# Kernel tuning notes

Measured on AMD Instinct MI355X. Metric: run time of the kernel, lower is better.

## Reference

```python
import jax, jax.numpy as jnp
import numpy as np

IN_F, HID, OUT_F = 227, 1024, 227
BATCH, SEQ_LEN = 256, 100
COND_NUM, GT_NUM = 5, 5


def _condition_lst(seq_len, condition_num=COND_NUM, groundtruth_num=GT_NUM):
    gt = np.ones((100, groundtruth_num))
    con = np.zeros((100, condition_num))
    lst = np.concatenate((gt, con), 1).reshape(-1)
    return lst[:seq_len].astype(bool)


def _lstm_cell(x, h, c, Wih, Whh, bih, bhh):
    gates = x @ Wih.T + bih + h @ Whh.T + bhh  # [B, 4H]
    i, f, g, o = jnp.split(gates, 4, axis=-1)
    c_new = jax.nn.sigmoid(f) * c + jax.nn.sigmoid(i) * jnp.tanh(g)
    h_new = jax.nn.sigmoid(o) * jnp.tanh(c_new)
    return h_new, c_new


def setup_inputs() -> dict:
    key = jax.random.key(0)
    ks = jax.random.split(key, 16)
    s = 0.03
    inp = {"real_seq": jax.random.normal(ks[0], (BATCH, SEQ_LEN, IN_F), jnp.float32)}
    shapes = {
        "Wih1": (4 * HID, IN_F), "Whh1": (4 * HID, HID), "bih1": (4 * HID,), "bhh1": (4 * HID,),
        "Wih2": (4 * HID, HID), "Whh2": (4 * HID, HID), "bih2": (4 * HID,), "bhh2": (4 * HID,),
        "Wih3": (4 * HID, HID), "Whh3": (4 * HID, HID), "bih3": (4 * HID,), "bhh3": (4 * HID,),
        "Wd": (OUT_F, HID), "bd": (OUT_F,),
    }
    for i, (name, shp) in enumerate(shapes.items()):
        inp[name] = jax.random.normal(ks[i + 1], shp, jnp.float32) * s
    return inp


def reference(real_seq, Wih1, Whh1, bih1, bhh1, Wih2, Whh2, bih2, bhh2,
              Wih3, Whh3, bih3, bhh3, Wd, bd):
    batch, seq_len, _ = real_seq.shape
    cond = jnp.asarray(_condition_lst(seq_len))  # [T] bool, True -> teacher forcing
    zeros_h = jnp.zeros((batch, HID), real_seq.dtype)
    out0 = jnp.zeros((batch, OUT_F), real_seq.dtype)
    carry0 = (zeros_h, zeros_h, zeros_h, zeros_h, zeros_h, zeros_h, out0)

    def step(carry, xs):
        h0, h1, h2, c0, c1, c2, prev_out = carry
        gt_frame, use_gt = xs
        in_frame = jnp.where(use_gt, gt_frame, prev_out)
        # NOTE: faithful to the original quirk — lstm2/lstm3 consume the OLD
        # h0 / h1 (pre-update), not the freshly computed ones.
        h0n, c0n = _lstm_cell(in_frame, h0, c0, Wih1, Whh1, bih1, bhh1)
        h1n, c1n = _lstm_cell(h0, h1, c1, Wih2, Whh2, bih2, bhh2)
        h2n, c2n = _lstm_cell(h1, h2, c2, Wih3, Whh3, bih3, bhh3)
        out_frame = h2n @ Wd.T + bd
        return (h0n, h1n, h2n, c0n, c1n, c2n, out_frame), out_frame

    xs = (jnp.transpose(real_seq, (1, 0, 2)), cond)  # [T,B,F], [T]
    _, out_frames = jax.lax.scan(step, carry0, xs)   # [T,B,OUT_F]
    out_seq = jnp.transpose(out_frames, (1, 0, 2)).reshape(batch, seq_len * OUT_F)
    return out_seq
```

## Files before the change

### kernel.cpp

```cpp
#include <hip/hip_runtime.h>
#include <cstdint>

typedef _Float16 f16;
typedef _Float16 f16x8 __attribute__((ext_vector_type(8)));
typedef float    f32x4 __attribute__((ext_vector_type(4)));

#define DINL __device__ __forceinline__

static constexpr int HID = 1024;
static constexpr int NG  = 4096;
static constexpr int BB  = 256;
static constexpr int TT  = 100;
static constexpr int KX  = 256;
static constexpr size_t MSZ = (size_t)NG * HID;

static constexpr size_t OFF_PACKW5 = 0;
static constexpr size_t OFF_W1D    = OFF_PACKW5 + 5*MSZ*2;
static constexpr size_t OFF_WIH1   = OFF_W1D   + MSZ*2;
static constexpr size_t OFF_WD     = OFF_WIH1  + (size_t)NG*KX*2;
static constexpr size_t OFF_XPAD   = OFF_WD    + (size_t)256*HID*2;
static constexpr size_t OFF_BIAS   = OFF_XPAD  + (size_t)TT*BB*KX*2;
static constexpr size_t OFF_C      = OFF_BIAS  + (size_t)4*NG*4;
static constexpr size_t OFF_HBUF   = OFF_C     + (size_t)3*BB*HID*4;
static constexpr size_t OFF_H2Z    = OFF_HBUF  + (size_t)4*BB*HID*2;
static constexpr size_t OFF_H2ALL  = OFF_H2Z   + (size_t)BB*HID*2;

DINL void async16(void* lds, const void* g){
  auto lp = reinterpret_cast<__attribute__((address_space(3))) unsigned int*>(
      reinterpret_cast<uintptr_t>(lds));
  auto gp = reinterpret_cast<const __attribute__((address_space(1))) unsigned int*>(
      reinterpret_cast<uintptr_t>(g));
  __builtin_amdgcn_global_load_lds(gp, lp, 16, 0, 0);
}

DINL f16x8 ldsr128(unsigned a){
  f16x8 r;
  asm volatile("ds_read_b128 %0, %1" : "=v"(r) : "v"(a));
  return r;
}

DINL float sigf(float x){
  x = fminf(fmaxf(x, -30.f), 30.f);
  return __fdividef(1.f, 1.f + __expf(-x));
}
DINL float tanh_fast(float x){
  x = fminf(fmaxf(x, -15.f), 15.f);
  float t = __expf(2.f*x);
  return __fdividef(t - 1.f, t + 1.f);
}

DINL void gemm_tile(f32x4 acc[4][4],
                    const f16* __restrict__ A, int m0, int sA,
                    const f16* __restrict__ Bp, int n0, int K,
                    char* ldsA, char* ldsB, int w, int lane)
{
  const int m_w = (w>>1)*64, n_w = (w&1)*64, c15 = lane&15;
  for (int k0 = 0; k0 < K; k0 += 64){
    __syncthreads();
    #pragma unroll
    for (int q = 0; q < 4; q++){
      int r0  = w*32 + q*8;
      int row = r0 + (lane>>3);
      int kg  = (lane&7) ^ (row&7);
      async16(ldsA + r0*128, A  + (size_t)(m0+row)*sA + k0 + kg*8);
      async16(ldsB + r0*128, Bp + (size_t)(n0+row)*K  + k0 + kg*8);
    }
    __syncthreads();
    #pragma unroll
    for (int kw = 0; kw < 2; kw++){
      f16x8 af[4], bf[4];
      #pragma unroll
      for (int ti = 0; ti < 4; ti++){
        int row  = m_w + ti*16 + c15;
        int phys = (kw*4 + (lane>>4)) ^ (row&7);
        af[ti] = *(const f16x8*)(ldsA + row*128 + phys*16);
      }
      #pragma unroll
      for (int tj = 0; tj < 4; tj++){
        int row  = n_w + tj*16 + c15;
        int phys = (kw*4 + (lane>>4)) ^ (row&7);
        bf[tj] = *(const f16x8*)(ldsB + row*128 + phys*16);
      }
      #pragma unroll
      for (int ti = 0; ti < 4; ti++)
        #pragma unroll
        for (int tj = 0; tj < 4; tj++)
          acc[ti][tj] = __builtin_amdgcn_mfma_f32_16x16x32_f16(af[ti], bf[tj], acc[ti][tj], 0, 0, 0);
    }
  }
}


__global__ void k_pack5(const float* W0, const float* W1, const float* W2,
                        const float* W3, const float* W4, char* ws)
{
  f16* dst = (f16*)(ws + OFF_PACKW5);
  const int mat = blockIdx.y;
  const float* src = mat==0?W0 : mat==1?W1 : mat==2?W2 : mat==3?W3 : W4;
  int tid = blockIdx.x*256 + threadIdx.x;
  int n = tid >> 7, kc = tid & 127;
  int r = ((n&3) << 10) + (n >> 2);
  const float* s = src + (size_t)r*HID + kc*8;
  f16x8 o;
  #pragma unroll
  for (int i = 0; i < 8; i++) o[i] = (f16)s[i];
  *(f16x8*)(dst + (size_t)mat*MSZ + (size_t)n*HID + kc*8) = o;
}

__global__ void k_packwih1(const float* __restrict__ Wih1, char* ws){
  f16* dst = (f16*)(ws + OFF_WIH1);
  int n = blockIdx.x, k = threadIdx.x;
  int r = ((n&3) << 10) + (n >> 2);
  dst[(size_t)n*KX + k] = (k < 227) ? (f16)Wih1[(size_t)r*227 + k] : (f16)0.f;
}

__global__ void k_packwd(const float* __restrict__ Wd, char* ws){
  f16* dst = (f16*)(ws + OFF_WD);
  int o = blockIdx.x;
  #pragma unroll
  for (int j = 0; j < 4; j++){
    int k = threadIdx.x + j*256;
    dst[(size_t)o*HID + k] = (o < 227) ? (f16)Wd[(size_t)o*HID + k] : (f16)0.f;
  }
}

__global__ void k_packwdt(const float* __restrict__ Wd, char* ws){
  f16* dst = (f16*)(ws + OFF_H2ALL);
  int h = blockIdx.x, o = threadIdx.x;
  dst[(size_t)h*KX + o] = (o < 227) ? (f16)Wd[(size_t)o*HID + h] : (f16)0.f;
}

__global__ void k_xpad(const float* __restrict__ seq, char* ws){
  f16* dst = (f16*)(ws + OFF_XPAD);
  int idx = blockIdx.x*256 + threadIdx.x;
  int t = idx >> 16, rem = idx & 65535, b = rem >> 8, k = rem & 255;
  dst[idx] = (k < 227) ? (f16)seq[(size_t)b*22700 + (size_t)t*227 + k] : (f16)0.f;
}

__global__ void k_bias(const float* bih1, const float* bhh1, const float* bih2, const float* bhh2,
                       const float* bih3, const float* bhh3, const float* Wih1, const float* bd,
                       char* ws)
{
  int n = blockIdx.x*256 + threadIdx.x;
  if (n >= NG) return;
  int r = ((n&3) << 10) + (n >> 2);
  float* b = (float*)(ws + OFF_BIAS);
  float bf = bih1[r] + bhh1[r];
  float s = 0.f;
  for (int o = 0; o < 227; o++) s += Wih1[(size_t)r*227 + o] * bd[o];
  b[n]        = bf;
  b[NG + n]   = bf + s;
  b[2*NG + n] = bih2[r] + bhh2[r];
  b[3*NG + n] = bih3[r] + bhh3[r];
}

__global__ __launch_bounds__(256, 2) void k_w1d(char* ws)
{
  __shared__ __align__(16) char ldsA[16384];
  __shared__ __align__(16) char ldsB[16384];
  const int w = threadIdx.x >> 6, lane = threadIdx.x & 63;
  const int n0 = blockIdx.x*128, m0 = blockIdx.y*128;
  const f16* A  = (const f16*)(ws + OFF_WIH1);
  const f16* Bp = (const f16*)(ws + OFF_H2ALL);
  f16* W1D = (f16*)(ws + OFF_W1D);

  f32x4 acc[4][4];
  f32x4 zero = {0.f, 0.f, 0.f, 0.f};
  #pragma unroll
  for (int i = 0; i < 4; i++)
    #pragma unroll
    for (int j = 0; j < 4; j++) acc[i][j] = zero;

  gemm_tile(acc, A, m0, KX, Bp, n0, KX, ldsA, ldsB, w, lane);

  const int m_w = (w>>1)*64, n_w = (w&1)*64, quad = lane>>4, c15 = lane&15;
  #pragma unroll
  for (int tj = 0; tj < 4; tj++){
    int col = n0 + n_w + tj*16 + c15;
    #pragma unroll
    for (int ti = 0; ti < 4; ti++){
      f32x4 v = acc[ti][tj];
      #pragma unroll
      for (int r = 0; r < 4; r++){
        int m = m0 + m_w + ti*16 + quad*4 + r;
        W1D[(size_t)m*HID + col] = (f16)v[r];
      }
    }
  }
}

__global__ __launch_bounds__(512, 2) void k_step(char* __restrict__ ws, int t, int use_gt)
{
  __shared__ __align__(16) char lds[163840];
  const int w = threadIdx.x >> 6, lane = threadIdx.x & 63;
  const int col0 = blockIdx.x*64, layer = blockIdx.y;

  const f16* packW = (const f16*)(ws + OFF_PACKW5);
  const f16* W1D   = (const f16*)(ws + OFF_W1D);
  const f16* WIH1  = (const f16*)(ws + OFF_WIH1);
  const f16* XP    = (const f16*)(ws + OFF_XPAD) + (size_t)t*BB*KX;
  const float* biasb = (const float*)(ws + OFF_BIAS);
  float* Cst = (float*)(ws + OFF_C);
  f16* HB  = (f16*)(ws + OFF_HBUF);
  f16* H2Z = (f16*)(ws + OFF_H2Z);
  f16* H2A = (f16*)(ws + OFF_H2ALL);

  const int pr = t & 1, pw = pr ^ 1;
  const f16* h0p = HB + (size_t)(pr*2 + 0)*BB*HID;
  const f16* h1p = HB + (size_t)(pr*2 + 1)*BB*HID;
  const f16* h2p = (t == 0) ? H2Z : (H2A + (size_t)(t-1)*BB*HID);

  const f16 *A0, *A1, *B0, *B1; int K1, sA1;
  const float* biasp; f16* hout; float* cptr;
  if (layer == 0){
    A0 = h0p; B0 = packW;
    if (use_gt){ A1 = XP;  B1 = WIH1; K1 = KX;  sA1 = KX;  biasp = biasb; }
    else       { A1 = h2p; B1 = W1D;  K1 = HID; sA1 = HID; biasp = biasb + NG; }
    hout = HB + (size_t)(pw*2 + 0)*BB*HID; cptr = Cst;
  } else if (layer == 1){
    A0 = h0p; B0 = packW + MSZ;  A1 = h1p; B1 = packW + 2*MSZ; K1 = HID; sA1 = HID;
    biasp = biasb + 2*NG; hout = HB + (size_t)(pw*2 + 1)*BB*HID; cptr = Cst + (size_t)BB*HID;
  } else {
    A0 = h1p; B0 = packW + 3*MSZ; A1 = h2p; B1 = packW + 4*MSZ; K1 = HID; sA1 = HID;
    biasp = biasb + 3*NG; hout = H2A + (size_t)t*BB*HID; cptr = Cst + (size_t)2*BB*HID;
  }
  const int ncmax = 16 + (K1 >> 6);

  const int rsub = lane >> 3;
  const int kxe  = ((lane & 7) ^ rsub) * 8;

  auto issueA = [&](int cc, int buf){
    const f16* src; int strd;
    if (cc < 16){ src = A0 + (size_t)cc*64;      strd = HID; }
    else        { src = A1 + (size_t)(cc-16)*64; strd = sA1; }
    char* dst = lds + 65536 + w*12288 + buf*4096;
    #pragma unroll
    for (int q = 0; q < 4; q++)
      async16(dst + q*1024, src + (size_t)(w*32 + q*8 + rsub)*strd + kxe);
  };
  auto issueB = [&](int chunk, int j){
    const f16* src; int strd;
    if (chunk < 16){ src = B0 + (size_t)chunk*64;      strd = HID; }
    else           { src = B1 + (size_t)(chunk-16)*64; strd = K1;  }
    async16(lds + (chunk & 7)*8192 + j*1024,
            src + (size_t)(col0 + j*8 + rsub)*strd + kxe);
  };

  f32x4 acc[2][4];
  f32x4 zero = {0.f, 0.f, 0.f, 0.f};
  #pragma unroll
  for (int i = 0; i < 2; i++)
    #pragma unroll
    for (int j = 0; j < 4; j++) acc[i][j] = zero;

  const int m_w = w*32, c15 = lane&15, quad = lane>>4;

  const unsigned ldsBase = (unsigned)(uintptr_t)lds;
  const unsigned p0 = (unsigned)(( quad      ^ (c15&7)) * 16);
  const unsigned p1 = (unsigned)(((4 + quad) ^ (c15&7)) * 16);
  unsigned rA[2], rB[4];
  #pragma unroll
  for (int ti = 0; ti < 2; ti++) rA[ti] = (unsigned)((ti*16 + c15) * 128);
  #pragma unroll
  for (int tj = 0; tj < 4; tj++) rB[tj] = (unsigned)((tj*16 + c15) * 128);

  {
    const int cb = w >> 1, jb = (w & 1) * 4;
    #pragma unroll
    for (int k = 0; k < 4; k++) issueB(cb, jb + k);
  }
  issueA(0, 0); issueA(1, 1);

  int bR = 0, bW = 2;
  for (int c = 0; c < ncmax; c++){
    if (c == ncmax-1)                    asm volatile("s_waitcnt vmcnt(0)" ::: "memory");
    else if ((c&3)==0 || c >= ncmax-4)   asm volatile("s_waitcnt vmcnt(4)" ::: "memory");
    else                                 asm volatile("s_waitcnt vmcnt(5)" ::: "memory");
    if ((c & 3) == 0) __builtin_amdgcn_s_barrier();
    if (c <= ncmax-5) issueB(4*((c>>2)+1) + (w>>1), (w&1)*4 + (c&3));
    if (c <= ncmax-3) issueA(c+2, bW);

    const unsigned ab = ldsBase + 65536u + (unsigned)(w*12288) + (unsigned)(bR*4096);
    const unsigned bb = ldsBase + (unsigned)((c & 7) * 8192);

    f16x8 a0[2], b0[4], a1[2], b1[4];
    #pragma unroll
    for (int ti = 0; ti < 2; ti++) a0[ti] = ldsr128(ab + rA[ti] + p0);
    #pragma unroll
    for (int tj = 0; tj < 4; tj++) b0[tj] = ldsr128(bb + rB[tj] + p0);
    #pragma unroll
    for (int ti = 0; ti < 2; ti++) a1[ti] = ldsr128(ab + rA[ti] + p1);
    #pragma unroll
    for (int tj = 0; tj < 4; tj++) b1[tj] = ldsr128(bb + rB[tj] + p1);

    asm volatile("s_waitcnt lgkmcnt(6)"
      : "+v"(a0[0]), "+v"(a0[1]),
        "+v"(b0[0]), "+v"(b0[1]), "+v"(b0[2]), "+v"(b0[3]));
    #pragma unroll
    for (int ti = 0; ti < 2; ti++)
      #pragma unroll
      for (int tj = 0; tj < 4; tj++)
        acc[ti][tj] = __builtin_amdgcn_mfma_f32_16x16x32_f16(a0[ti], b0[tj], acc[ti][tj], 0, 0, 0);

    asm volatile("s_waitcnt lgkmcnt(0)"
      : "+v"(a1[0]), "+v"(a1[1]),
        "+v"(b1[0]), "+v"(b1[1]), "+v"(b1[2]), "+v"(b1[3]));
    #pragma unroll
    for (int ti = 0; ti < 2; ti++)
      #pragma unroll
      for (int tj = 0; tj < 4; tj++)
        acc[ti][tj] = __builtin_amdgcn_mfma_f32_16x16x32_f16(a1[ti], b1[tj], acc[ti][tj], 0, 0, 0);

    bR = (bR == 2) ? 0 : bR + 1;
    bW = (bW == 2) ? 0 : bW + 1;
  }

  const int gl = lane&3, sbase = lane&60;
  #pragma unroll
  for (int tj = 0; tj < 4; tj++){
    const int ncol = col0 + tj*16 + c15;
    const int unit = ncol >> 2;
    const float bn = biasp[ncol];
    float cp[8];
    #pragma unroll
    for (int ti = 0; ti < 2; ti++)
      #pragma unroll
      for (int r = 0; r < 4; r++)
        cp[ti*4 + r] = cptr[(size_t)(m_w + ti*16 + quad*4 + r)*HID + unit];
    #pragma unroll
    for (int ti = 0; ti < 2; ti++){
      f32x4 v = acc[ti][tj];
      #pragma unroll
      for (int r = 0; r < 4; r++){
        float x   = v[r] + bn;
        float act = (gl == 2) ? tanh_fast(x) : sigf(x);
        float iv = __shfl(act, sbase);
        float fv = __shfl(act, sbase + 1);
        float gv = __shfl(act, sbase + 2);
        float ov = __shfl(act, sbase + 3);
        float cn = fmaf(fv, cp[ti*4 + r], iv*gv);
        float hn = ov * tanh_fast(cn);
        int m = m_w + ti*16 + quad*4 + r;
        if (gl == 0)      cptr[(size_t)m*HID + unit] = cn;
        else if (gl == 1) hout[(size_t)m*HID + unit] = (f16)hn;
      }
    }
  }
}

__global__ __launch_bounds__(256, 2) void k_final(const char* __restrict__ ws,
                                                  const float* __restrict__ bd,
                                                  float* __restrict__ dout)
{
  __shared__ __align__(16) char ldsA[16384];
  __shared__ __align__(16) char ldsB[16384];
  const int w = threadIdx.x >> 6, lane = threadIdx.x & 63;
  const int n0 = blockIdx.x*128, m0 = blockIdx.y*128;
  const f16* A  = (const f16*)(ws + OFF_H2ALL);
  const f16* Bp = (const f16*)(ws + OFF_WD);

  f32x4 acc[4][4];
  f32x4 zero = {0.f, 0.f, 0.f, 0.f};
  #pragma unroll
  for (int i = 0; i < 4; i++)
    #pragma unroll
    for (int j = 0; j < 4; j++) acc[i][j] = zero;

  gemm_tile(acc, A, m0, HID, Bp, n0, HID, ldsA, ldsB, w, lane);

  const int m_w = (w>>1)*64, n_w = (w&1)*64, quad = lane>>4, c15 = lane&15;
  #pragma unroll
  for (int tj = 0; tj < 4; tj++){
    int o = n0 + n_w + tj*16 + c15;
    bool valid = (o < 227);
    float bn = valid ? bd[o] : 0.f;
    #pragma unroll
    for (int ti = 0; ti < 4; ti++){
      f32x4 v = acc[ti][tj];
      #pragma unroll
      for (int r = 0; r < 4; r++){
        int m = m0 + m_w + ti*16 + quad*4 + r;
        if (valid){
          int tt = m >> 8, b = m & 255;
          dout[(size_t)b*22700 + (size_t)tt*227 + o] = v[r] + bn;
        }
      }
    }
  }
}

extern "C" void kernel_launch(void* const* d_in, const int* in_sizes, int n_in,
                              void* d_out, int out_size, void* d_ws, size_t ws_size,
                              hipStream_t stream)
{
  (void)in_sizes; (void)n_in; (void)out_size; (void)ws_size;
  const float* seq  = (const float*)d_in[0];
  const float* Wih1 = (const float*)d_in[1];
  const float* Whh1 = (const float*)d_in[2];
  const float* bih1 = (const float*)d_in[3];
  const float* bhh1 = (const float*)d_in[4];
  const float* Wih2 = (const float*)d_in[5];
  const float* Whh2 = (const float*)d_in[6];
  const float* bih2 = (const float*)d_in[7];
  const float* bhh2 = (const float*)d_in[8];
  const float* Wih3 = (const float*)d_in[9];
  const float* Whh3 = (const float*)d_in[10];
  const float* bih3 = (const float*)d_in[11];
  const float* bhh3 = (const float*)d_in[12];
  const float* Wd   = (const float*)d_in[13];
  const float* bd   = (const float*)d_in[14];
  char* ws = (char*)d_ws;

  hipMemsetAsync(ws + OFF_C,    0, (size_t)3*BB*HID*4, stream);
  hipMemsetAsync(ws + OFF_HBUF, 0, (size_t)2*BB*HID*2, stream);
  hipMemsetAsync(ws + OFF_H2Z,  0, (size_t)BB*HID*2,   stream);

  k_pack5   <<<dim3(2048, 5), dim3(256), 0, stream>>>(Whh1, Wih2, Whh2, Wih3, Whh3, ws);
  k_packwih1<<<dim3(4096),    dim3(256), 0, stream>>>(Wih1, ws);
  k_packwd  <<<dim3(256),     dim3(256), 0, stream>>>(Wd, ws);
  k_packwdt <<<dim3(1024),    dim3(256), 0, stream>>>(Wd, ws);
  k_xpad    <<<dim3(25600),   dim3(256), 0, stream>>>(seq, ws);
  k_bias    <<<dim3(16),      dim3(256), 0, stream>>>(bih1, bhh1, bih2, bhh2, bih3, bhh3, Wih1, bd, ws);
  k_w1d     <<<dim3(8, 32),   dim3(256), 0, stream>>>(ws);

  for (int t = 0; t < TT; t++){
    int ug = ((t % 10) < 5) ? 1 : 0;
    k_step<<<dim3(64, 3), dim3(512), 0, stream>>>(ws, t, ug);
  }

  k_final<<<dim3(2, 200), dim3(256), 0, stream>>>((const char*)ws, bd, (float*)d_out);
}
```

Baseline: 3.191 ms.

## Fuse per-timestep launches into one persistent cooperative kernel with grid sync

Replaces the 100 per-timestep k_step launches with one cooperative kernel that loops over time and uses grid.sync between steps. Cell state now stays in registers instead of global memory, and biases are loaded once. The first B chunk for the next step is prefetched before the epilogue, and the B-tile issue schedule is regrouped per four-chunk group. This removes launch overhead and c-state traffic, but 192 blocks of 512 threads with 160KB LDS must all be co-resident for the cooperative launch, and grid barriers have their own cost.

```diff
diff --git a/kernel.cpp b/kernel.cpp
--- a/kernel.cpp
+++ b/kernel.cpp
@@ -1,5 +1,8 @@
 #include <hip/hip_runtime.h>
+#include <hip/hip_cooperative_groups.h>
 #include <cstdint>
+
+namespace cg = cooperative_groups;
 
 typedef _Float16 f16;
 typedef _Float16 f16x8 __attribute__((ext_vector_type(8)));
@@ -189,71 +192,43 @@
   }
 }
 
-__global__ __launch_bounds__(512, 2) void k_step(char* __restrict__ ws, int t, int use_gt)
+__global__ __launch_bounds__(512, 2) void k_steps(char* __restrict__ ws)
 {
   __shared__ __align__(16) char lds[163840];
+  cg::grid_group grid = cg::this_grid();
+
   const int w = threadIdx.x >> 6, lane = threadIdx.x & 63;
   const int col0 = blockIdx.x*64, layer = blockIdx.y;
 
   const f16* packW = (const f16*)(ws + OFF_PACKW5);
   const f16* W1D   = (const f16*)(ws + OFF_W1D);
   const f16* WIH1  = (const f16*)(ws + OFF_WIH1);
-  const f16* XP    = (const f16*)(ws + OFF_XPAD) + (size_t)t*BB*KX;
+  const f16* XPb   = (const f16*)(ws + OFF_XPAD);
   const float* biasb = (const float*)(ws + OFF_BIAS);
-  float* Cst = (float*)(ws + OFF_C);
   f16* HB  = (f16*)(ws + OFF_HBUF);
   f16* H2Z = (f16*)(ws + OFF_H2Z);
   f16* H2A = (f16*)(ws + OFF_H2ALL);
 
-  const int pr = t & 1, pw = pr ^ 1;
-  const f16* h0p = HB + (size_t)(pr*2 + 0)*BB*HID;
-  const f16* h1p = HB + (size_t)(pr*2 + 1)*BB*HID;
-  const f16* h2p = (t == 0) ? H2Z : (H2A + (size_t)(t-1)*BB*HID);
-
-  const f16 *A0, *A1, *B0, *B1; int K1, sA1;
-  const float* biasp; f16* hout; float* cptr;
-  if (layer == 0){
-    A0 = h0p; B0 = packW;
-    if (use_gt){ A1 = XP;  B1 = WIH1; K1 = KX;  sA1 = KX;  biasp = biasb; }
-    else       { A1 = h2p; B1 = W1D;  K1 = HID; sA1 = HID; biasp = biasb + NG; }
-    hout = HB + (size_t)(pw*2 + 0)*BB*HID; cptr = Cst;
-  } else if (layer == 1){
-    A0 = h0p; B0 = packW + MSZ;  A1 = h1p; B1 = packW + 2*MSZ; K1 = HID; sA1 = HID;
-    biasp = biasb + 2*NG; hout = HB + (size_t)(pw*2 + 1)*BB*HID; cptr = Cst + (size_t)BB*HID;
-  } else {
-    A0 = h1p; B0 = packW + 3*MSZ; A1 = h2p; B1 = packW + 4*MSZ; K1 = HID; sA1 = HID;
-    biasp = biasb + 3*NG; hout = H2A + (size_t)t*BB*HID; cptr = Cst + (size_t)2*BB*HID;
-  }
-  const int ncmax = 16 + (K1 >> 6);
+  const f16* B0 = (layer==0) ? packW : (layer==1) ? packW + MSZ : packW + 3*MSZ;
+  const f16* B1h = (layer==0) ? W1D  : (layer==1) ? packW + 2*MSZ : packW + 4*MSZ;
 
   const int rsub = lane >> 3;
   const int kxe  = ((lane & 7) ^ rsub) * 8;
-
-  auto issueA = [&](int cc, int buf){
-    const f16* src; int strd;
-    if (cc < 16){ src = A0 + (size_t)cc*64;      strd = HID; }
-    else        { src = A1 + (size_t)(cc-16)*64; strd = sA1; }
-    char* dst = lds + 65536 + w*12288 + buf*4096;
-    #pragma unroll
-    for (int q = 0; q < 4; q++)
-      async16(dst + q*1024, src + (size_t)(w*32 + q*8 + rsub)*strd + kxe);
-  };
-  auto issueB = [&](int chunk, int j){
-    const f16* src; int strd;
-    if (chunk < 16){ src = B0 + (size_t)chunk*64;      strd = HID; }
-    else           { src = B1 + (size_t)(chunk-16)*64; strd = K1;  }
-    async16(lds + (chunk & 7)*8192 + j*1024,
-            src + (size_t)(col0 + j*8 + rsub)*strd + kxe);
-  };
-
-  f32x4 acc[2][4];
-  f32x4 zero = {0.f, 0.f, 0.f, 0.f};
-  #pragma unroll
-  for (int i = 0; i < 2; i++)
-    #pragma unroll
-    for (int j = 0; j < 4; j++) acc[i][j] = zero;
-
   const int m_w = w*32, c15 = lane&15, quad = lane>>4;
+
+  const float* bsel0 = (layer==0) ? biasb        : (layer==1) ? biasb + 2*NG : biasb + 3*NG;
+  const float* bsel1 = (layer==0) ? biasb + NG   : bsel0;
+  float bgt[4], bngt[4];
+  #pragma unroll
+  for (int tj = 0; tj < 4; tj++){
+    int ncol = col0 + tj*16 + c15;
+    bgt[tj]  = bsel0[ncol];
+    bngt[tj] = bsel1[ncol];
+  }
+
+  float creg[32];
+  #pragma unroll
+  for (int i = 0; i < 32; i++) creg[i] = 0.f;
 
   const unsigned ldsBase = (unsigned)(uintptr_t)lds;
   const unsigned p0 = (unsigned)(( quad      ^ (c15&7)) * 16);
@@ -265,86 +240,153 @@
   for (int tj = 0; tj < 4; tj++) rB[tj] = (unsigned)((tj*16 + c15) * 128);
 
   {
-    const int cb = w >> 1, jb = (w & 1) * 4;
-    #pragma unroll
-    for (int k = 0; k < 4; k++) issueB(cb, jb + k);
-  }
-  issueA(0, 0); issueA(1, 1);
-
-  int bR = 0, bW = 2;
-  for (int c = 0; c < ncmax; c++){
-    if (c == ncmax-1)                    asm volatile("s_waitcnt vmcnt(0)" ::: "memory");
-    else if ((c&3)==0 || c >= ncmax-4)   asm volatile("s_waitcnt vmcnt(4)" ::: "memory");
-    else                                 asm volatile("s_waitcnt vmcnt(5)" ::: "memory");
-    if ((c & 3) == 0) __builtin_amdgcn_s_barrier();
-    if (c <= ncmax-5) issueB(4*((c>>2)+1) + (w>>1), (w&1)*4 + (c&3));
-    if (c <= ncmax-3) issueA(c+2, bW);
-
-    const unsigned ab = ldsBase + 65536u + (unsigned)(w*12288) + (unsigned)(bR*4096);
-    const unsigned bb = ldsBase + (unsigned)((c & 7) * 8192);
-
-    f16x8 a0[2], b0[4], a1[2], b1[4];
-    #pragma unroll
-    for (int ti = 0; ti < 2; ti++) a0[ti] = ldsr128(ab + rA[ti] + p0);
-    #pragma unroll
-    for (int tj = 0; tj < 4; tj++) b0[tj] = ldsr128(bb + rB[tj] + p0);
-    #pragma unroll
-    for (int ti = 0; ti < 2; ti++) a1[ti] = ldsr128(ab + rA[ti] + p1);
-    #pragma unroll
-    for (int tj = 0; tj < 4; tj++) b1[tj] = ldsr128(bb + rB[tj] + p1);
-
-    asm volatile("s_waitcnt lgkmcnt(6)"
-      : "+v"(a0[0]), "+v"(a0[1]),
-        "+v"(b0[0]), "+v"(b0[1]), "+v"(b0[2]), "+v"(b0[3]));
-    #pragma unroll
-    for (int ti = 0; ti < 2; ti++)
-      #pragma unroll
-      for (int tj = 0; tj < 4; tj++)
-        acc[ti][tj] = __builtin_amdgcn_mfma_f32_16x16x32_f16(a0[ti], b0[tj], acc[ti][tj], 0, 0, 0);
-
-    asm volatile("s_waitcnt lgkmcnt(0)"
-      : "+v"(a1[0]), "+v"(a1[1]),
-        "+v"(b1[0]), "+v"(b1[1]), "+v"(b1[2]), "+v"(b1[3]));
-    #pragma unroll
-    for (int ti = 0; ti < 2; ti++)
-      #pragma unroll
-      for (int tj = 0; tj < 4; tj++)
-        acc[ti][tj] = __builtin_amdgcn_mfma_f32_16x16x32_f16(a1[ti], b1[tj], acc[ti][tj], 0, 0, 0);
-
-    bR = (bR == 2) ? 0 : bR + 1;
-    bW = (bW == 2) ? 0 : bW + 1;
-  }
-
-  const int gl = lane&3, sbase = lane&60;
-  #pragma unroll
-  for (int tj = 0; tj < 4; tj++){
-    const int ncol = col0 + tj*16 + c15;
-    const int unit = ncol >> 2;
-    const float bn = biasp[ncol];
-    float cp[8];
-    #pragma unroll
-    for (int ti = 0; ti < 2; ti++)
-      #pragma unroll
-      for (int r = 0; r < 4; r++)
-        cp[ti*4 + r] = cptr[(size_t)(m_w + ti*16 + quad*4 + r)*HID + unit];
-    #pragma unroll
-    for (int ti = 0; ti < 2; ti++){
-      f32x4 v = acc[ti][tj];
-      #pragma unroll
-      for (int r = 0; r < 4; r++){
-        float x   = v[r] + bn;
-        float act = (gl == 2) ? tanh_fast(x) : sigf(x);
-        float iv = __shfl(act, sbase);
-        float fv = __shfl(act, sbase + 1);
-        float gv = __shfl(act, sbase + 2);
-        float ov = __shfl(act, sbase + 3);
-        float cn = fmaf(fv, cp[ti*4 + r], iv*gv);
-        float hn = ov * tanh_fast(cn);
-        int m = m_w + ti*16 + quad*4 + r;
-        if (gl == 0)      cptr[(size_t)m*HID + unit] = cn;
-        else if (gl == 1) hout[(size_t)m*HID + unit] = (f16)hn;
-      }
-    }
+    const int chunk = w >> 1, jb = (w & 1) * 4;
+    #pragma unroll
+    for (int k = 0; k < 4; k++){
+      int j = jb + k;
+      async16(lds + (chunk & 7)*8192 + j*1024,
+              B0 + (size_t)chunk*64 + (size_t)(col0 + j*8 + rsub)*HID + kxe);
+    }
+  }
+
+  for (int t = 0; t < TT; t++){
+    const int use_gt = ((t % 10) < 5) ? 1 : 0;
+    const int pr = t & 1, pw = pr ^ 1;
+    const f16* h0p = HB + (size_t)(pr*2 + 0)*BB*HID;
+    const f16* h1p = HB + (size_t)(pr*2 + 1)*BB*HID;
+    const f16* h2p = (t == 0) ? H2Z : (H2A + (size_t)(t-1)*BB*HID);
+
+    const f16 *A0, *A1, *B1; int K1, sA1; f16* hout;
+    if (layer == 0){
+      A0 = h0p;
+      if (use_gt){ A1 = XPb + (size_t)t*BB*KX; B1 = WIH1; K1 = KX;  sA1 = KX;  }
+      else       { A1 = h2p;                   B1 = B1h;  K1 = HID; sA1 = HID; }
+      hout = HB + (size_t)(pw*2 + 0)*BB*HID;
+    } else if (layer == 1){
+      A0 = h0p; A1 = h1p; B1 = B1h; K1 = HID; sA1 = HID;
+      hout = HB + (size_t)(pw*2 + 1)*BB*HID;
+    } else {
+      A0 = h1p; A1 = h2p; B1 = B1h; K1 = HID; sA1 = HID;
+      hout = H2A + (size_t)t*BB*HID;
+    }
+    const int ncmax = 16 + (K1 >> 6);
+    const int lastg = (ncmax >> 2) - 1;
+
+    auto issueA = [&](int cc, int buf){
+      const f16* src; int strd;
+      if (cc < 16){ src = A0 + (size_t)cc*64;      strd = HID; }
+      else        { src = A1 + (size_t)(cc-16)*64; strd = sA1; }
+      char* dst = lds + 65536 + w*12288 + buf*4096;
+      #pragma unroll
+      for (int q = 0; q < 4; q++)
+        async16(dst + q*1024, src + (size_t)(w*32 + q*8 + rsub)*strd + kxe);
+    };
+    auto issueB = [&](int chunk, int j){
+      const f16* src; int strd;
+      if (chunk < 16){ src = B0 + (size_t)chunk*64;      strd = HID; }
+      else           { src = B1 + (size_t)(chunk-16)*64; strd = K1;  }
+      async16(lds + (chunk & 7)*8192 + j*1024,
+              src + (size_t)(col0 + j*8 + rsub)*strd + kxe);
+    };
+
+    f32x4 acc[2][4];
+    f32x4 zero = {0.f, 0.f, 0.f, 0.f};
+    #pragma unroll
+    for (int i = 0; i < 2; i++)
+      #pragma unroll
+      for (int j = 0; j < 4; j++) acc[i][j] = zero;
+
+    issueA(0, 0); issueA(1, 1);
+
+    int bR = 0, bW = 2;
+    for (int c = 0; c < ncmax; c++){
+      if (c == ncmax-1)                        asm volatile("s_waitcnt vmcnt(0)" ::: "memory");
+      else if ((c&3)==1 && c < ncmax-4)        asm volatile("s_waitcnt vmcnt(8)" ::: "memory");
+      else                                     asm volatile("s_waitcnt vmcnt(4)" ::: "memory");
+      if ((c & 3) == 0){
+        __builtin_amdgcn_s_barrier();
+        const int g1 = (c >> 2) + 1;
+        if (g1 <= lastg){
+          const int chunk = 4*g1 + (w >> 1), jb = (w & 1) * 4;
+          #pragma unroll
+          for (int k = 0; k < 4; k++) issueB(chunk, jb + k);
+        }
+      }
+      if (c <= ncmax-3) issueA(c+2, bW);
+
+      const unsigned ab = ldsBase + 65536u + (unsigned)(w*12288) + (unsigned)(bR*4096);
+      const unsigned bb = ldsBase + (unsigned)((c & 7) * 8192);
+
+      f16x8 a0[2], b0[4], a1[2], b1[4];
+      #pragma unroll
+      for (int ti = 0; ti < 2; ti++) a0[ti] = ldsr128(ab + rA[ti] + p0);
+      #pragma unroll
+      for (int tj = 0; tj < 4; tj++) b0[tj] = ldsr128(bb + rB[tj] + p0);
+      #pragma unroll
+      for (int ti = 0; ti < 2; ti++) a1[ti] = ldsr128(ab + rA[ti] + p1);
+      #pragma unroll
+      for (int tj = 0; tj < 4; tj++) b1[tj] = ldsr128(bb + rB[tj] + p1);
+
+      asm volatile("s_waitcnt lgkmcnt(6)"
+        : "+v"(a0[0]), "+v"(a0[1]),
+          "+v"(b0[0]), "+v"(b0[1]), "+v"(b0[2]), "+v"(b0[3]));
+      #pragma unroll
+      for (int ti = 0; ti < 2; ti++)
+        #pragma unroll
+        for (int tj = 0; tj < 4; tj++)
+          acc[ti][tj] = __builtin_amdgcn_mfma_f32_16x16x32_f16(a0[ti], b0[tj], acc[ti][tj], 0, 0, 0);
+
+      asm volatile("s_waitcnt lgkmcnt(0)"
+        : "+v"(a1[0]), "+v"(a1[1]),
+          "+v"(b1[0]), "+v"(b1[1]), "+v"(b1[2]), "+v"(b1[3]));
+      #pragma unroll
+      for (int ti = 0; ti < 2; ti++)
+        #pragma unroll
+        for (int tj = 0; tj < 4; tj++)
+          acc[ti][tj] = __builtin_amdgcn_mfma_f32_16x16x32_f16(a1[ti], b1[tj], acc[ti][tj], 0, 0, 0);
+
+      bR = (bR == 2) ? 0 : bR + 1;
+      bW = (bW == 2) ? 0 : bW + 1;
+    }
+
+    __builtin_amdgcn_s_barrier();
+    if (t + 1 < TT){
+      const int chunk = w >> 1, jb = (w & 1) * 4;
+      #pragma unroll
+      for (int k = 0; k < 4; k++){
+        int j = jb + k;
+        async16(lds + (chunk & 7)*8192 + j*1024,
+                B0 + (size_t)chunk*64 + (size_t)(col0 + j*8 + rsub)*HID + kxe);
+      }
+    }
+
+    const int gl = lane&3, sbase = lane&60;
+    #pragma unroll
+    for (int tj = 0; tj < 4; tj++){
+      const int ncol = col0 + tj*16 + c15;
+      const int unit = ncol >> 2;
+      const float bn = use_gt ? bgt[tj] : bngt[tj];
+      #pragma unroll
+      for (int ti = 0; ti < 2; ti++){
+        f32x4 v = acc[ti][tj];
+        #pragma unroll
+        for (int r = 0; r < 4; r++){
+          float x   = v[r] + bn;
+          float act = (gl == 2) ? tanh_fast(x) : sigf(x);
+          float iv = __shfl(act, sbase);
+          float fv = __shfl(act, sbase + 1);
+          float gv = __shfl(act, sbase + 2);
+          float ov = __shfl(act, sbase + 3);
+          float cn = fmaf(fv, creg[tj*8 + ti*4 + r], iv*gv);
+          creg[tj*8 + ti*4 + r] = cn;
+          float hn = ov * tanh_fast(cn);
+          int m = m_w + ti*16 + quad*4 + r;
+          if (gl == 1) hout[(size_t)m*HID + unit] = (f16)hn;
+        }
+      }
+    }
+
+    if (t + 1 < TT) grid.sync();
   }
 }
 
@@ -411,7 +453,6 @@
   const float* bd   = (const float*)d_in[14];
   char* ws = (char*)d_ws;
 
-  hipMemsetAsync(ws + OFF_C,    0, (size_t)3*BB*HID*4, stream);
   hipMemsetAsync(ws + OFF_HBUF, 0, (size_t)2*BB*HID*2, stream);
   hipMemsetAsync(ws + OFF_H2Z,  0, (size_t)BB*HID*2,   stream);
 
@@ -423,10 +464,9 @@
   k_bias    <<<dim3(16),      dim3(256), 0, stream>>>(bih1, bhh1, bih2, bhh2, bih3, bhh3, Wih1, bd, ws);
   k_w1d     <<<dim3(8, 32),   dim3(256), 0, stream>>>(ws);
 
-  for (int t = 0; t < TT; t++){
-    int ug = ((t % 10) < 5) ? 1 : 0;
-    k_step<<<dim3(64, 3), dim3(512), 0, stream>>>(ws, t, ug);
-  }
+  char* wsp = ws;
+  void* kargs[] = { (void*)&wsp };
+  hipLaunchCooperativeKernel((const void*)k_steps, dim3(64, 3), dim3(512), kargs, 0, stream);
 
   k_final<<<dim3(2, 200), dim3(256), 0, stream>>>((const char*)ws, bd, (float*)d_out);
 }
```

Result: slower. 5.003 ms (+56.8%).

## Load B weight fragments directly into registers, drop LDS staging for B

Applied to the files above, without the earlier changes.

The weight (B) operand is now loaded straight from global memory into registers with global_load_dwordx4 in MFMA fragment layout, with a 4-deep register ring buffer, instead of being staged through LDS. Only the A (activation) tiles still go through LDS, now in per-wave 4-slot buffers with a deeper prefetch, and the LDS allocation shrinks. This removes LDS write/read traffic and most block barriers for B, at the cost of many more VGPRs (32 f16x8 registers for B buffers), uncoalesced-looking strided global reads per lane, and redundant B loads across the 8 waves that share the same columns.

```diff
diff --git a/kernel.cpp b/kernel.cpp
--- a/kernel.cpp
+++ b/kernel.cpp
@@ -36,6 +36,13 @@
 DINL f16x8 ldsr128(unsigned a){
   f16x8 r;
   asm volatile("ds_read_b128 %0, %1" : "=v"(r) : "v"(a));
+  return r;
+}
+
+DINL f16x8 gload(unsigned voff, const f16* sbase){
+  f16x8 r;
+  asm volatile("global_load_dwordx4 %0, %1, %2"
+    : "=v"(r) : "v"(voff), "s"(sbase));
   return r;
 }
 
@@ -191,7 +198,7 @@
 
 __global__ __launch_bounds__(512, 2) void k_step(char* __restrict__ ws, int t, int use_gt)
 {
-  __shared__ __align__(16) char lds[163840];
+  __shared__ __align__(16) char lds[131072];
   const int w = threadIdx.x >> 6, lane = threadIdx.x & 63;
   const int col0 = blockIdx.x*64, layer = blockIdx.y;
 
@@ -228,22 +235,43 @@
 
   const int rsub = lane >> 3;
   const int kxe  = ((lane & 7) ^ rsub) * 8;
-
-  auto issueA = [&](int cc, int buf){
+  const int m_w = w*32, c15 = lane&15, quad = lane>>4;
+
+  auto issueA = [&](int ci, int buf){
     const f16* src; int strd;
-    if (cc < 16){ src = A0 + (size_t)cc*64;      strd = HID; }
-    else        { src = A1 + (size_t)(cc-16)*64; strd = sA1; }
-    char* dst = lds + 65536 + w*12288 + buf*4096;
+    if (ci < 16){ src = A0 + (size_t)ci*64;      strd = HID; }
+    else        { src = A1 + (size_t)(ci-16)*64; strd = sA1; }
+    char* dst = lds + w*16384 + buf*4096;
     #pragma unroll
     for (int q = 0; q < 4; q++)
       async16(dst + q*1024, src + (size_t)(w*32 + q*8 + rsub)*strd + kxe);
   };
-  auto issueB = [&](int chunk, int j){
-    const f16* src; int strd;
-    if (chunk < 16){ src = B0 + (size_t)chunk*64;      strd = HID; }
-    else           { src = B1 + (size_t)(chunk-16)*64; strd = K1;  }
-    async16(lds + (chunk & 7)*8192 + j*1024,
-            src + (size_t)(col0 + j*8 + rsub)*strd + kxe);
+
+  const f16* sb0[4]; const f16* sb1[4];
+  #pragma unroll
+  for (int tj = 0; tj < 4; tj++){
+    sb0[tj] = B0 + (size_t)(col0 + tj*16)*HID;
+    sb1[tj] = B1 + (size_t)(col0 + tj*16)*K1;
+  }
+  const unsigned vB0 = (unsigned)(c15*HID*2 + quad*16);
+  const unsigned vB1 = (unsigned)(c15*K1*2  + quad*16);
+
+  auto issueB = [&](int ci, f16x8* bf){
+    if (ci < 16){
+      const int ko = ci*64;
+      #pragma unroll
+      for (int tj = 0; tj < 4; tj++){
+        bf[tj*2+0] = gload(vB0, sb0[tj] + ko);
+        bf[tj*2+1] = gload(vB0, sb0[tj] + ko + 32);
+      }
+    } else {
+      const int ko = (ci-16)*64;
+      #pragma unroll
+      for (int tj = 0; tj < 4; tj++){
+        bf[tj*2+0] = gload(vB1, sb1[tj] + ko);
+        bf[tj*2+1] = gload(vB1, sb1[tj] + ko + 32);
+      }
+    }
   };
 
   f32x4 acc[2][4];
@@ -252,68 +280,60 @@
   for (int i = 0; i < 2; i++)
     #pragma unroll
     for (int j = 0; j < 4; j++) acc[i][j] = zero;
-
-  const int m_w = w*32, c15 = lane&15, quad = lane>>4;
 
   const unsigned ldsBase = (unsigned)(uintptr_t)lds;
   const unsigned p0 = (unsigned)(( quad      ^ (c15&7)) * 16);
   const unsigned p1 = (unsigned)(((4 + quad) ^ (c15&7)) * 16);
-  unsigned rA[2], rB[4];
-  #pragma unroll
-  for (int ti = 0; ti < 2; ti++) rA[ti] = (unsigned)((ti*16 + c15) * 128);
-  #pragma unroll
-  for (int tj = 0; tj < 4; tj++) rB[tj] = (unsigned)((tj*16 + c15) * 128);
-
-  {
-    const int cb = w >> 1, jb = (w & 1) * 4;
-    #pragma unroll
-    for (int k = 0; k < 4; k++) issueB(cb, jb + k);
-  }
-  issueA(0, 0); issueA(1, 1);
-
-  int bR = 0, bW = 2;
-  for (int c = 0; c < ncmax; c++){
-    if (c == ncmax-1)                    asm volatile("s_waitcnt vmcnt(0)" ::: "memory");
-    else if ((c&3)==0 || c >= ncmax-4)   asm volatile("s_waitcnt vmcnt(4)" ::: "memory");
-    else                                 asm volatile("s_waitcnt vmcnt(5)" ::: "memory");
-    if ((c & 3) == 0) __builtin_amdgcn_s_barrier();
-    if (c <= ncmax-5) issueB(4*((c>>2)+1) + (w>>1), (w&1)*4 + (c&3));
-    if (c <= ncmax-3) issueA(c+2, bW);
-
-    const unsigned ab = ldsBase + 65536u + (unsigned)(w*12288) + (unsigned)(bR*4096);
-    const unsigned bb = ldsBase + (unsigned)((c & 7) * 8192);
-
-    f16x8 a0[2], b0[4], a1[2], b1[4];
-    #pragma unroll
-    for (int ti = 0; ti < 2; ti++) a0[ti] = ldsr128(ab + rA[ti] + p0);
-    #pragma unroll
-    for (int tj = 0; tj < 4; tj++) b0[tj] = ldsr128(bb + rB[tj] + p0);
-    #pragma unroll
-    for (int ti = 0; ti < 2; ti++) a1[ti] = ldsr128(ab + rA[ti] + p1);
-    #pragma unroll
-    for (int tj = 0; tj < 4; tj++) b1[tj] = ldsr128(bb + rB[tj] + p1);
-
-    asm volatile("s_waitcnt lgkmcnt(6)"
-      : "+v"(a0[0]), "+v"(a0[1]),
-        "+v"(b0[0]), "+v"(b0[1]), "+v"(b0[2]), "+v"(b0[3]));
-    #pragma unroll
-    for (int ti = 0; ti < 2; ti++)
-      #pragma unroll
-      for (int tj = 0; tj < 4; tj++)
-        acc[ti][tj] = __builtin_amdgcn_mfma_f32_16x16x32_f16(a0[ti], b0[tj], acc[ti][tj], 0, 0, 0);
-
-    asm volatile("s_waitcnt lgkmcnt(0)"
-      : "+v"(a1[0]), "+v"(a1[1]),
-        "+v"(b1[0]), "+v"(b1[1]), "+v"(b1[2]), "+v"(b1[3]));
-    #pragma unroll
-    for (int ti = 0; ti < 2; ti++)
-      #pragma unroll
-      for (int tj = 0; tj < 4; tj++)
-        acc[ti][tj] = __builtin_amdgcn_mfma_f32_16x16x32_f16(a1[ti], b1[tj], acc[ti][tj], 0, 0, 0);
-
-    bR = (bR == 2) ? 0 : bR + 1;
-    bW = (bW == 2) ? 0 : bW + 1;
-  }
+  const unsigned rA0 = (unsigned)((c15) * 128);
+  const unsigned rA1 = (unsigned)((16 + c15) * 128);
+
+  f16x8 bbuf[4][8];
+
+  issueA(0, 0); issueB(0, bbuf[0]);
+  issueA(1, 1); issueB(1, bbuf[1]);
+  issueA(2, 2); issueB(2, bbuf[2]);
+  issueA(3, 3); issueB(3, bbuf[3]);
+
+#define WAITVM(N, BF) asm volatile("s_waitcnt vmcnt(" #N ")" \
+    : "+v"(BF[0]), "+v"(BF[1]), "+v"(BF[2]), "+v"(BF[3]),    \
+      "+v"(BF[4]), "+v"(BF[5]), "+v"(BF[6]), "+v"(BF[7]))
+
+#define S_COMPUTE(KK)                                                         \
+    const unsigned ab = ldsBase + (unsigned)(w*16384) + (KK*4096u);           \
+    f16x8 a0[2], a1[2];                                                       \
+    a0[0] = ldsr128(ab + rA0 + p0);                                           \
+    a0[1] = ldsr128(ab + rA1 + p0);                                           \
+    a1[0] = ldsr128(ab + rA0 + p1);                                           \
+    a1[1] = ldsr128(ab + rA1 + p1);                                           \
+    asm volatile("s_waitcnt lgkmcnt(2)" : "+v"(a0[0]), "+v"(a0[1]));          \
+    _Pragma("unroll")                                                         \
+    for (int ti = 0; ti < 2; ti++)                                            \
+      _Pragma("unroll")                                                       \
+      for (int tj = 0; tj < 4; tj++)                                          \
+        acc[ti][tj] = __builtin_amdgcn_mfma_f32_16x16x32_f16(                 \
+            a0[ti], bbuf[KK][tj*2+0], acc[ti][tj], 0, 0, 0);                  \
+    asm volatile("s_waitcnt lgkmcnt(0)" : "+v"(a1[0]), "+v"(a1[1]));          \
+    _Pragma("unroll")                                                         \
+    for (int ti = 0; ti < 2; ti++)                                            \
+      _Pragma("unroll")                                                       \
+      for (int tj = 0; tj < 4; tj++)                                          \
+        acc[ti][tj] = __builtin_amdgcn_mfma_f32_16x16x32_f16(                 \
+            a1[ti], bbuf[KK][tj*2+1], acc[ti][tj], 0, 0, 0);
+
+  for (int c0 = 0; c0 + 4 < ncmax; c0 += 4){
+    if ((c0 & 7) == 0) __builtin_amdgcn_s_barrier();
+    { WAITVM(36, bbuf[0]); S_COMPUTE(0); issueA(c0+4, 0); issueB(c0+4, bbuf[0]); }
+    { WAITVM(36, bbuf[1]); S_COMPUTE(1); issueA(c0+5, 1); issueB(c0+5, bbuf[1]); }
+    { WAITVM(36, bbuf[2]); S_COMPUTE(2); issueA(c0+6, 2); issueB(c0+6, bbuf[2]); }
+    { WAITVM(36, bbuf[3]); S_COMPUTE(3); issueA(c0+7, 3); issueB(c0+7, bbuf[3]); }
+  }
+  { WAITVM(36, bbuf[0]); S_COMPUTE(0); }
+  { WAITVM(24, bbuf[1]); S_COMPUTE(1); }
+  { WAITVM(12, bbuf[2]); S_COMPUTE(2); }
+  { WAITVM(0,  bbuf[3]); S_COMPUTE(3); }
+
+#undef S_COMPUTE
+#undef WAITVM
 
   const int gl = lane&3, sbase = lane&60;
   #pragma unroll
```

Measured after the change: 7.617 ms. +138.7%, slower.

## Software-pipeline LDS fragment loads one chunk ahead with deeper async prefetch

Applied to the files above, without the earlier changes.

Restructures the GEMM main loop so the LDS-to-register fragment reads for chunk c+1 are issued before the MFMAs of chunk c, using double-buffered register fragments. A and B global-to-LDS prefetch move one stage deeper: three A buffers are in flight and B is issued in groups of four per 4-chunk group with a barrier. The loop is manually unrolled by four, with hand-tuned vmcnt/lgkmcnt waits and explicit prologue and epilogue chunks. The goal is to hide LDS read latency behind MFMA work. The cost is roughly doubled fragment register use, which may hurt occupancy, and fragile waitcnt accounting.

```diff
diff --git a/kernel.cpp b/kernel.cpp
--- a/kernel.cpp
+++ b/kernel.cpp
@@ -228,11 +228,12 @@
 
   const int rsub = lane >> 3;
   const int kxe  = ((lane & 7) ^ rsub) * 8;
-
-  auto issueA = [&](int cc, int buf){
+  const int m_w = w*32, c15 = lane&15, quad = lane>>4;
+
+  auto issueA = [&](int ci, int buf){
     const f16* src; int strd;
-    if (cc < 16){ src = A0 + (size_t)cc*64;      strd = HID; }
-    else        { src = A1 + (size_t)(cc-16)*64; strd = sA1; }
+    if (ci < 16){ src = A0 + (size_t)ci*64;      strd = HID; }
+    else        { src = A1 + (size_t)(ci-16)*64; strd = sA1; }
     char* dst = lds + 65536 + w*12288 + buf*4096;
     #pragma unroll
     for (int q = 0; q < 4; q++)
@@ -253,67 +254,125 @@
     #pragma unroll
     for (int j = 0; j < 4; j++) acc[i][j] = zero;
 
-  const int m_w = w*32, c15 = lane&15, quad = lane>>4;
-
   const unsigned ldsBase = (unsigned)(uintptr_t)lds;
+  const unsigned aBase   = ldsBase + 65536u + (unsigned)(w*12288);
   const unsigned p0 = (unsigned)(( quad      ^ (c15&7)) * 16);
   const unsigned p1 = (unsigned)(((4 + quad) ^ (c15&7)) * 16);
-  unsigned rA[2], rB[4];
-  #pragma unroll
-  for (int ti = 0; ti < 2; ti++) rA[ti] = (unsigned)((ti*16 + c15) * 128);
-  #pragma unroll
-  for (int tj = 0; tj < 4; tj++) rB[tj] = (unsigned)((tj*16 + c15) * 128);
+  const unsigned rA0 = (unsigned)(( 0 + c15) * 128);
+  const unsigned rA1 = (unsigned)((16 + c15) * 128);
+  const unsigned rB0 = (unsigned)(( 0 + c15) * 128);
+  const unsigned rB1 = (unsigned)((16 + c15) * 128);
+  const unsigned rB2 = (unsigned)((32 + c15) * 128);
+  const unsigned rB3 = (unsigned)((48 + c15) * 128);
+
+  f16x8 fA0[2][2], fB0[2][4], fA1[2][2], fB1[2][4];
+
+#define DS12(NX)                                                   \
+    { const unsigned sN = ldsBase + (unsigned)((((c+1)&7))*8192);  \
+      const unsigned aN = aBase + (unsigned)(bufN*4096);           \
+      fA0[NX][0] = ldsr128(aN + rA0 + p0);                         \
+      fA0[NX][1] = ldsr128(aN + rA1 + p0);                         \
+      fB0[NX][0] = ldsr128(sN + rB0 + p0);                         \
+      fB0[NX][1] = ldsr128(sN + rB1 + p0);                         \
+      fB0[NX][2] = ldsr128(sN + rB2 + p0);                         \
+      fB0[NX][3] = ldsr128(sN + rB3 + p0);                         \
+      fA1[NX][0] = ldsr128(aN + rA0 + p1);                         \
+      fA1[NX][1] = ldsr128(aN + rA1 + p1);                         \
+      fB1[NX][0] = ldsr128(sN + rB0 + p1);                         \
+      fB1[NX][1] = ldsr128(sN + rB1 + p1);                         \
+      fB1[NX][2] = ldsr128(sN + rB2 + p1);                         \
+      fB1[NX][3] = ldsr128(sN + rB3 + p1); }
+
+#define TIES(BK) "+v"(fA0[BK][0]), "+v"(fA0[BK][1]),               \
+    "+v"(fB0[BK][0]), "+v"(fB0[BK][1]), "+v"(fB0[BK][2]), "+v"(fB0[BK][3]), \
+    "+v"(fA1[BK][0]), "+v"(fA1[BK][1]),                            \
+    "+v"(fB1[BK][0]), "+v"(fB1[BK][1]), "+v"(fB1[BK][2]), "+v"(fB1[BK][3])
+
+#define MFMA16(BK)                                                 \
+    _Pragma("unroll")                                              \
+    for (int ti = 0; ti < 2; ti++)                                 \
+      _Pragma("unroll")                                            \
+      for (int tj = 0; tj < 4; tj++)                               \
+        acc[ti][tj] = __builtin_amdgcn_mfma_f32_16x16x32_f16(      \
+            fA0[BK][ti], fB0[BK][tj], acc[ti][tj], 0, 0, 0);       \
+    _Pragma("unroll")                                              \
+    for (int ti = 0; ti < 2; ti++)                                 \
+      _Pragma("unroll")                                            \
+      for (int tj = 0; tj < 4; tj++)                               \
+        acc[ti][tj] = __builtin_amdgcn_mfma_f32_16x16x32_f16(      \
+            fA1[BK][ti], fB1[BK][tj], acc[ti][tj], 0, 0, 0);
+
+#define ADV { bufA = bufN; bufN = (bufN==2)?0:bufN+1; ++c; }
+
+#define ITER_N(VMN, CUR, NX)                                       \
+  { asm volatile("s_waitcnt vmcnt(" #VMN ")" ::: "memory");        \
+    DS12(NX);                                                      \
+    asm volatile("s_waitcnt lgkmcnt(12)" : TIES(CUR));             \
+    issueA(c+3, bufA);                                             \
+    MFMA16(CUR); ADV; }
+
+#define ITER_X(CUR, NX)                                            \
+  { asm volatile("s_waitcnt vmcnt(4)" ::: "memory");               \
+    asm volatile("s_waitcnt lgkmcnt(0)" : TIES(CUR));              \
+    __builtin_amdgcn_s_barrier();                                  \
+    __builtin_amdgcn_sched_barrier(0);                             \
+    DS12(NX);                                                      \
+    if (c <= ncmax-9){                                             \
+      const int ch = 4*(((c+1)>>2)+1) + (w>>1), jb = (w&1)*4;      \
+      issueB(ch, jb+0); issueB(ch, jb+1);                          \
+      issueB(ch, jb+2); issueB(ch, jb+3);                          \
+    }                                                              \
+    issueA(c+3, bufA);                                             \
+    MFMA16(CUR); ADV; }
 
   {
-    const int cb = w >> 1, jb = (w & 1) * 4;
+    const int jb = (w & 1) * 4, cb = w >> 1;
     #pragma unroll
     for (int k = 0; k < 4; k++) issueB(cb, jb + k);
-  }
-  issueA(0, 0); issueA(1, 1);
-
-  int bR = 0, bW = 2;
-  for (int c = 0; c < ncmax; c++){
-    if (c == ncmax-1)                    asm volatile("s_waitcnt vmcnt(0)" ::: "memory");
-    else if ((c&3)==0 || c >= ncmax-4)   asm volatile("s_waitcnt vmcnt(4)" ::: "memory");
-    else                                 asm volatile("s_waitcnt vmcnt(5)" ::: "memory");
-    if ((c & 3) == 0) __builtin_amdgcn_s_barrier();
-    if (c <= ncmax-5) issueB(4*((c>>2)+1) + (w>>1), (w&1)*4 + (c&3));
-    if (c <= ncmax-3) issueA(c+2, bW);
-
-    const unsigned ab = ldsBase + 65536u + (unsigned)(w*12288) + (unsigned)(bR*4096);
-    const unsigned bb = ldsBase + (unsigned)((c & 7) * 8192);
-
-    f16x8 a0[2], b0[4], a1[2], b1[4];
-    #pragma unroll
-    for (int ti = 0; ti < 2; ti++) a0[ti] = ldsr128(ab + rA[ti] + p0);
-    #pragma unroll
-    for (int tj = 0; tj < 4; tj++) b0[tj] = ldsr128(bb + rB[tj] + p0);
-    #pragma unroll
-    for (int ti = 0; ti < 2; ti++) a1[ti] = ldsr128(ab + rA[ti] + p1);
-    #pragma unroll
-    for (int tj = 0; tj < 4; tj++) b1[tj] = ldsr128(bb + rB[tj] + p1);
-
-    asm volatile("s_waitcnt lgkmcnt(6)"
-      : "+v"(a0[0]), "+v"(a0[1]),
-        "+v"(b0[0]), "+v"(b0[1]), "+v"(b0[2]), "+v"(b0[3]));
-    #pragma unroll
-    for (int ti = 0; ti < 2; ti++)
-      #pragma unroll
-      for (int tj = 0; tj < 4; tj++)
-        acc[ti][tj] = __builtin_amdgcn_mfma_f32_16x16x32_f16(a0[ti], b0[tj], acc[ti][tj], 0, 0, 0);
-
-    asm volatile("s_waitcnt lgkmcnt(0)"
-      : "+v"(a1[0]), "+v"(a1[1]),
-        "+v"(b1[0]), "+v"(b1[1]), "+v"(b1[2]), "+v"(b1[3]));
-    #pragma unroll
-    for (int ti = 0; ti < 2; ti++)
-      #pragma unroll
-      for (int tj = 0; tj < 4; tj++)
-        acc[ti][tj] = __builtin_amdgcn_mfma_f32_16x16x32_f16(a1[ti], b1[tj], acc[ti][tj], 0, 0, 0);
-
-    bR = (bR == 2) ? 0 : bR + 1;
-    bW = (bW == 2) ? 0 : bW + 1;
-  }
+    #pragma unroll
+    for (int k = 0; k < 4; k++) issueB(4 + cb, jb + k);
+  }
+  issueA(0, 0); issueA(1, 1); issueA(2, 2);
+  asm volatile("s_waitcnt vmcnt(8)" ::: "memory");
+  __builtin_amdgcn_s_barrier();
+  __builtin_amdgcn_sched_barrier(0);
+
+  int c = -1, bufA = 0, bufN = 0;
+  DS12(0);
+  c = 0; bufA = 0; bufN = 1;
+
+  ITER_N(4, 0, 1)
+  ITER_N(4, 1, 0)
+  ITER_N(4, 0, 1)
+  ITER_X(   1, 0)
+  for (int g = 1; g <= (ncmax >> 2) - 2; ++g){
+    ITER_N(8, 0, 1)
+    ITER_N(4, 1, 0)
+    ITER_N(4, 0, 1)
+    ITER_X(   1, 0)
+  }
+  { asm volatile("s_waitcnt vmcnt(4)" ::: "memory");
+    DS12(1);
+    asm volatile("s_waitcnt lgkmcnt(12)" : TIES(0));
+    issueA(c+3, bufA);
+    MFMA16(0); ADV; }
+  { asm volatile("s_waitcnt vmcnt(4)" ::: "memory");
+    DS12(0);
+    asm volatile("s_waitcnt lgkmcnt(12)" : TIES(1));
+    MFMA16(1); ADV; }
+  { asm volatile("s_waitcnt vmcnt(0)" ::: "memory");
+    DS12(1);
+    asm volatile("s_waitcnt lgkmcnt(12)" : TIES(0));
+    MFMA16(0); ADV; }
+  { asm volatile("s_waitcnt lgkmcnt(0)" : TIES(1));
+    MFMA16(1); }
+
+#undef ITER_X
+#undef ITER_N
+#undef ADV
+#undef MFMA16
+#undef TIES
+#undef DS12
 
   const int gl = lane&3, sbase = lane&60;
   #pragma unroll
```

Measured after the change: 3.115 ms. 2.4% less time.
